# Performance work log

Measured on AMD Instinct MI355X. Metric: run time of the kernel, lower is better.

Reference implementation:

```python
import jax, jax.numpy as jnp
import numpy as np

D_MODEL = 4096
N_HEADS = 32
KV_HEADS = 8
HEAD_DIM = D_MODEL // N_HEADS  # 128
GROUPS = N_HEADS // KV_HEADS   # 4
ROPE_THETA = 500000.0
CLIP_QKV = 8.0
SEQLENS = [512, 768, 384, 384]
T = sum(SEQLENS)  # 2048 total ragged tokens


def setup_inputs() -> dict:
    key = jax.random.key(0)
    k1, k2, k3 = jax.random.split(key, 3)
    hidden_states = jax.random.normal(k1, (T, D_MODEL), dtype=jnp.float32)
    # fused Wqkv: rows = d_model (Q) + 2 * kv_heads * head_dim (K,V)
    w_qkv = jax.random.normal(k2, (D_MODEL + 2 * KV_HEADS * HEAD_DIM, D_MODEL), dtype=jnp.float32) * 0.02
    w_o = jax.random.normal(k3, (D_MODEL, D_MODEL), dtype=jnp.float32) * 0.02
    # ragged-batch metadata: cumulative sequence lengths, per-token positions
    cu = np.concatenate([[0], np.cumsum(SEQLENS)]).astype(np.int32)
    pos = np.concatenate([np.arange(l) for l in SEQLENS]).astype(np.float32)
    inv_freq = 1.0 / (ROPE_THETA ** (np.arange(0, HEAD_DIM, 2, dtype=np.float32) / HEAD_DIM))  # [64]
    freqs = pos[:, None] * inv_freq[None, :]  # [T, 64]
    return {
        "hidden_states": hidden_states,
        "w_qkv": w_qkv,
        "w_o": w_o,
        "cos": jnp.asarray(np.cos(freqs), dtype=jnp.float32),
        "sin": jnp.asarray(np.sin(freqs), dtype=jnp.float32),
        "cu_seqlens": jnp.asarray(cu),
    }


def _rope(x, cos, sin):
    # rotate-half (NeoX-style) RoPE, as in TGI PositionRotaryEmbedding
    h = HEAD_DIM // 2
    x1, x2 = x[..., :h], x[..., h:]
    c = cos[:, None, :]  # [T,1,h] broadcast over heads
    s = sin[:, None, :]
    return jnp.concatenate([x1 * c - x2 * s, x2 * c + x1 * s], axis=-1)


def reference(hidden_states, w_qkv, w_o, cos, sin, cu_seqlens):
    # fused QKV projection + clip_qkv clamp
    qkv = jnp.clip(hidden_states @ w_qkv.T, -CLIP_QKV, CLIP_QKV)  # [T, 6144]
    q_sz = N_HEADS * HEAD_DIM
    kv_sz = KV_HEADS * HEAD_DIM
    q = qkv[:, :q_sz].reshape(T, N_HEADS, HEAD_DIM)
    k = qkv[:, q_sz:q_sz + kv_sz].reshape(T, KV_HEADS, HEAD_DIM)
    v = qkv[:, q_sz + kv_sz:].reshape(T, KV_HEADS, HEAD_DIM)
    q = _rope(q, cos, sin)
    k = _rope(k, cos, sin)
    # GQA: expand kv heads to query heads (kv_head_mapping = repeat_interleave)
    kr = jnp.repeat(k, GROUPS, axis=1)  # [T, H, D]
    vr = jnp.repeat(v, GROUPS, axis=1)
    # varlen causal mask: same segment AND key index <= query index
    idx = jnp.arange(T)
    seg = jnp.searchsorted(cu_seqlens, idx, side="right") - 1  # [T]
    mask = (seg[:, None] == seg[None, :]) & (idx[:, None] >= idx[None, :])  # [T,T]
    scale = HEAD_DIM ** -0.5
    scores = jnp.einsum("qhd,khd->hqk", q, kr) * scale  # [H,T,T]
    scores = jnp.where(mask[None, :, :], scores, jnp.finfo(scores.dtype).min)
    attn = jax.nn.softmax(scores, axis=-1)
    out = jnp.einsum("hqk,khd->qhd", attn, vr).reshape(T, N_HEADS * HEAD_DIM)
    return out @ w_o.T
```

## Files before the change

### kernel.cpp

```cpp
#include <hip/hip_runtime.h>

#define T_TOK 2048
#define DM    4096
#define NH    32
#define KVH   8
#define HD    128
#define QKV_N 6144
#define KOFF  4096
#define VOFF  5120
#define SCALE 0.08838834764831845f

typedef __attribute__((ext_vector_type(8))) short  short8;
typedef __attribute__((ext_vector_type(4))) float  floatx4;

__device__ __forceinline__ ushort f2bf(float f) {
  union { float f; unsigned u; } x; x.f = f;
  unsigned u = x.u;
  return (ushort)((u + 0x7fffu + ((u >> 16) & 1u)) >> 16);
}
__device__ __forceinline__ float bf2f(ushort h) {
  union { unsigned u; float f; } x; x.u = ((unsigned)h) << 16;
  return x.f;
}

__global__ void __launch_bounds__(256) cast_bf16_kernel(const float* __restrict__ x,
                                                        ushort* __restrict__ y, int n4) {
  int i = blockIdx.x * 256 + threadIdx.x;
  if (i >= n4) return;
  float4 v = ((const float4*)x)[i];
  ushort4 o;
  o.x = f2bf(v.x); o.y = f2bf(v.y); o.z = f2bf(v.z); o.w = f2bf(v.w);
  ((ushort4*)y)[i] = o;
}

__global__ void __launch_bounds__(256) add_f32_kernel(const float4* __restrict__ a,
                                                      const float4* __restrict__ b,
                                                      float4* __restrict__ o, int n4) {
  int i = blockIdx.x * 256 + threadIdx.x;
  if (i >= n4) return;
  float4 x = a[i], y = b[i];
  o[i] = make_float4(x.x + y.x, x.y + y.y, x.z + y.z, x.w + y.w);
}

__device__ __forceinline__ void gld_lds16(const ushort* g, ushort* l) {
  __builtin_amdgcn_global_load_lds((const __attribute__((address_space(1))) unsigned int*)g,
                                   (__attribute__((address_space(3))) unsigned int*)l,
                                   16, 0, 0);
}

template <int MLO, int NLO>
__device__ __forceinline__ void mfma_quad(floatx4 (&acc)[8][4],
                                          const short8 (&afr)[4][2],
                                          const short8 (&bfr)[4][2]) {
  __builtin_amdgcn_s_setprio(1);
#pragma unroll
  for (int ks = 0; ks < 2; ++ks)
#pragma unroll
    for (int mi = 0; mi < 4; ++mi)
#pragma unroll
      for (int ni = 0; ni < 2; ++ni)
        acc[MLO + mi][NLO + ni] = __builtin_amdgcn_mfma_f32_16x16x32_bf16(
            afr[mi][ks], bfr[NLO + ni][ks], acc[MLO + mi][NLO + ni], 0, 0, 0);
  __builtin_amdgcn_s_setprio(0);
}

__device__ __forceinline__ void stage_half(const ushort* __restrict__ G, size_t row0,
                                           int K, int k0, ushort* lbase, int tid) {
#pragma unroll
  for (int j = 0; j < 2; ++j) {
    int row   = j * 64 + (tid >> 3);
    int chunk = (tid & 7) ^ (row & 7);
    gld_lds16(G + (row0 + (size_t)row) * K + k0 + chunk * 8,
              lbase + (size_t)(j * 512 + tid) * 8);
  }
}

#define TILE(BUF, tt)                                                             \
  do {                                                                            \
    const ushort* Ab = (BUF) ? Ab1 : Ab0;                                         \
    const ushort* Bb = (BUF) ? Bb1 : Bb0;                                         \
        \
    _Pragma("unroll") for (int ni = 0; ni < 2; ++ni)                              \
      _Pragma("unroll") for (int ks = 0; ks < 2; ++ks)                            \
        bfr[ni][ks] = *(const short8*)&Bb[(brow + ni * 16 + r) * 64 +             \
                                          ((ks * 32 + g * 8) ^ cswz)];            \
    _Pragma("unroll") for (int m = 0; m < 4; ++m)                                 \
      _Pragma("unroll") for (int ks = 0; ks < 2; ++ks)                            \
        afr[m][ks] = *(const short8*)&Ab[(m * 16 + r) * 64 +                      \
                                         ((ks * 32 + g * 8) ^ cswz)];             \
    if ((tt) + 1 < NT)                                                            \
      stage_half(A, bm + 128, K, koff + ((tt) + 1) * 64,                          \
                 &As[1 - (BUF)][1][0][0], tid);                                   \
    __builtin_amdgcn_s_barrier();                                                 \
    mfma_quad<0, 0>(acc, afr, bfr);                                               \
    __builtin_amdgcn_s_barrier();                                                 \
        \
    _Pragma("unroll") for (int ni = 2; ni < 4; ++ni)                              \
      _Pragma("unroll") for (int ks = 0; ks < 2; ++ks)                            \
        bfr[ni][ks] = *(const short8*)&Bb[(brow + ni * 16 + r) * 64 +             \
                                          ((ks * 32 + g * 8) ^ cswz)];            \
    __builtin_amdgcn_s_barrier();                                                 \
    mfma_quad<0, 2>(acc, afr, bfr);                                               \
    __builtin_amdgcn_s_barrier();                                                 \
        \
    _Pragma("unroll") for (int m = 0; m < 4; ++m)                                 \
      _Pragma("unroll") for (int ks = 0; ks < 2; ++ks)                            \
        afr[m][ks] = *(const short8*)&Ab[((64 + m * 16) + r) * 64 +               \
                                         ((ks * 32 + g * 8) ^ cswz)];             \
    if ((tt) + 2 < NT)                                                            \
      stage_half(B, bn, K, koff + ((tt) + 2) * 64, &Bs[BUF][0][0][0], tid);       \
    __builtin_amdgcn_s_barrier();                                                 \
    mfma_quad<4, 2>(acc, afr, bfr);                                               \
    __builtin_amdgcn_s_barrier();                                                 \
        \
    if ((tt) + 2 < NT) {                                                          \
      stage_half(B, bn + 128, K, koff + ((tt) + 2) * 64, &Bs[BUF][1][0][0], tid); \
      stage_half(A, bm, K, koff + ((tt) + 2) * 64, &As[BUF][0][0][0], tid);       \
    }                                                                             \
    if ((tt) < NT - 2) asm volatile("s_waitcnt vmcnt(6)");                        \
    else               asm volatile("s_waitcnt vmcnt(0)");                        \
    __builtin_amdgcn_s_barrier();                                                 \
    mfma_quad<4, 0>(acc, afr, bfr);                                               \
    __builtin_amdgcn_s_barrier();                                                 \
  } while (0)

__global__ void __launch_bounds__(512, 2)
gemm256(const ushort* __restrict__ A, const ushort* __restrict__ B,
        ushort* __restrict__ Cb, float* __restrict__ Cf,
        int N, int K, int Kloc, int KS, int mode) {
  __shared__ __align__(16) ushort As[2][2][128][64];
  __shared__ __align__(16) ushort Bs[2][2][128][64];

  const int tid = threadIdx.x;
  const int lane = tid & 63, wv = tid >> 6;
  const int r = lane & 15, g = lane >> 4;
  const int wm = wv >> 2, wn = wv & 3;

  const int nwg = (int)gridDim.x;
  const int wg  = (int)blockIdx.x;
  const int wgs = (wg & 7) * (nwg >> 3) + (wg >> 3);
  const int nbx = N >> 8;
  const int by  = wgs / (nbx * KS);
  const int rem = wgs - by * nbx * KS;
  const int bx  = rem / KS;
  const int ks_ = rem - bx * KS;
  const int bm = by * 256, bn = bx * 256;
  const int koff = ks_ * Kloc;

  const int NT = Kloc >> 6;

  floatx4 acc[8][4];
#pragma unroll
  for (int mi = 0; mi < 8; ++mi)
#pragma unroll
    for (int ni = 0; ni < 4; ++ni) acc[mi][ni] = (floatx4){0.f, 0.f, 0.f, 0.f};

  stage_half(B, bn,       K, koff, &Bs[0][0][0][0], tid);
  stage_half(B, bn + 128, K, koff, &Bs[0][1][0][0], tid);
  stage_half(A, bm,       K, koff, &As[0][0][0][0], tid);
  stage_half(A, bm + 128, K, koff, &As[0][1][0][0], tid);
  if (NT > 1) {
    stage_half(B, bn,       K, koff + 64, &Bs[1][0][0][0], tid);
    stage_half(B, bn + 128, K, koff + 64, &Bs[1][1][0][0], tid);
    stage_half(A, bm,       K, koff + 64, &As[1][0][0][0], tid);
    asm volatile("s_waitcnt vmcnt(6)");
  } else {
    asm volatile("s_waitcnt vmcnt(0)");
  }
  __builtin_amdgcn_s_barrier();

  short8 afr[4][2], bfr[4][2];
  const int cswz = (r & 7) << 3;
  const int brow = (wn & 1) * 64;
  const ushort* Ab0 = &As[0][wm][0][0];
  const ushort* Ab1 = &As[1][wm][0][0];
  const ushort* Bb0 = &Bs[0][wn >> 1][0][0];
  const ushort* Bb1 = &Bs[1][wn >> 1][0][0];

  for (int t = 0; t < NT; t += 2) {
    TILE(0, t);
    TILE(1, t + 1);
  }

  float* Cfo = Cf + (size_t)ks_ * ((size_t)2048 * N);
#pragma unroll
  for (int mi = 0; mi < 8; ++mi)
#pragma unroll
    for (int v = 0; v < 4; ++v) {
      int row = bm + wm * 128 + mi * 16 + g * 4 + v;
#pragma unroll
      for (int ni = 0; ni < 4; ++ni) {
        int col = bn + wn * 64 + ni * 16 + r;
        float x = acc[mi][ni][v];
        if (mode == 0) {
          x = fminf(8.0f, fmaxf(-8.0f, x));
          Cb[(size_t)row * N + col] = f2bf(x);
        } else {
          Cfo[(size_t)row * N + col] = x;
        }
      }
    }
}

__global__ void __launch_bounds__(256) rope_kernel(ushort* __restrict__ qkv,
                                                   const float* __restrict__ cosb,
                                                   const float* __restrict__ sinb) {
  int t = blockIdx.y;
  int h = blockIdx.x * 4 + (threadIdx.x >> 6);
  int d = threadIdx.x & 63;
  size_t base = (size_t)t * QKV_N + (h < NH ? h * HD : KOFF + (h - NH) * HD);
  float x1 = bf2f(qkv[base + d]);
  float x2 = bf2f(qkv[base + 64 + d]);
  float c = cosb[t * 64 + d], s = sinb[t * 64 + d];
  float y1 = x1 * c - x2 * s;
  float y2 = x2 * c + x1 * s;
  if (h < NH) { y1 *= SCALE; y2 *= SCALE; }
  qkv[base + d]      = f2bf(y1);
  qkv[base + 64 + d] = f2bf(y2);
}

__global__ void __launch_bounds__(256) vtrans_kernel(const ushort* __restrict__ qkv,
                                                     ushort* __restrict__ vt) {
  int idx = blockIdx.x * 256 + threadIdx.x;
  int t  = idx & (T_TOK - 1);
  int d  = (idx >> 11) & (HD - 1);
  int kv = idx >> 18;
  vt[idx] = qkv[(size_t)t * QKV_N + VOFF + kv * HD + d];
}

__global__ void __launch_bounds__(256) attn_kernel(const ushort* __restrict__ qkv,
                                                   const ushort* __restrict__ vt,
                                                   ushort* __restrict__ o) {
  __shared__ ushort Ks[64][136];
  __shared__ ushort Vts[128][72];
  __shared__ ushort Ps[4][16][72];

  const int tid = threadIdx.x, wave = tid >> 6, lane = tid & 63;
  const int r = lane & 15, g = lane >> 4;
  const int qtile = blockIdx.x, head = blockIdx.y, kvh = head >> 2;
  const int q0 = qtile * 64;
  int s0;
  if (q0 < 512) s0 = 0; else if (q0 < 1280) s0 = 512;
  else if (q0 < 1664) s0 = 1280; else s0 = 1664;

  short8 qf[4];
  const int qrow = q0 + wave * 16 + r;
#pragma unroll
  for (int ks = 0; ks < 4; ks++)
    qf[ks] = *(const short8*)&qkv[(size_t)qrow * QKV_N + head * HD + ks * 32 + g * 8];

  floatx4 zero = {0.f, 0.f, 0.f, 0.f};
  floatx4 oacc[8];
#pragma unroll
  for (int b = 0; b < 8; b++) oacc[b] = zero;
  float mrun[4] = {-1e30f, -1e30f, -1e30f, -1e30f};
  float lrun[4] = {0.f, 0.f, 0.f, 0.f};

  const size_t kcol  = (size_t)KOFF + kvh * HD;
  const size_t vbase = (size_t)kvh * HD * T_TOK;

  for (int k0 = s0; k0 < q0 + 64; k0 += 64) {
    short8 kreg[4], vreg[4];
#pragma unroll
    for (int p = 0; p < 4; p++) {
      int krow = p * 16 + (tid >> 4), kc = (tid & 15) * 8;
      kreg[p] = *(const short8*)&qkv[(size_t)(k0 + krow) * QKV_N + kcol + kc];
      int vd = p * 32 + (tid >> 3), vc = (tid & 7) * 8;
      vreg[p] = *(const short8*)&vt[vbase + (size_t)vd * T_TOK + k0 + vc];
    }
    __syncthreads();
#pragma unroll
    for (int p = 0; p < 4; p++) {
      int krow = p * 16 + (tid >> 4), kc = (tid & 15) * 8;
      *(short8*)&Ks[krow][kc] = kreg[p];
      int vd = p * 32 + (tid >> 3), vc = (tid & 7) * 8;
      *(short8*)&Vts[vd][vc] = vreg[p];
    }
    __syncthreads();

    floatx4 sacc[4];
#pragma unroll
    for (int s = 0; s < 4; s++) sacc[s] = zero;
#pragma unroll
    for (int s = 0; s < 4; s++)
#pragma unroll
      for (int ks = 0; ks < 4; ks++) {
        short8 kf = *(const short8*)&Ks[s * 16 + r][ks * 32 + g * 8];
        sacc[s] = __builtin_amdgcn_mfma_f32_16x16x32_bf16(qf[ks], kf, sacc[s], 0, 0, 0);
      }

    const bool diag = (k0 == q0);
    float sv[4][4];
#pragma unroll
    for (int s = 0; s < 4; s++)
#pragma unroll
      for (int v = 0; v < 4; v++) {
        float x = sacc[s][v];
        if (diag) {
          int ka = k0 + s * 16 + r;
          int qa = q0 + wave * 16 + g * 4 + v;
          if (ka > qa) x = -1e30f;
        }
        sv[s][v] = x;
      }

    float rmax[4];
#pragma unroll
    for (int v = 0; v < 4; v++)
      rmax[v] = fmaxf(fmaxf(sv[0][v], sv[1][v]), fmaxf(sv[2][v], sv[3][v]));
#pragma unroll
    for (int off = 1; off < 16; off <<= 1)
#pragma unroll
      for (int v = 0; v < 4; v++)
        rmax[v] = fmaxf(rmax[v], __shfl_xor(rmax[v], off, 64));

    float newm[4], alpha[4];
#pragma unroll
    for (int v = 0; v < 4; v++) {
      newm[v]  = fmaxf(mrun[v], rmax[v]);
      alpha[v] = __expf(mrun[v] - newm[v]);
      mrun[v]  = newm[v];
    }

    float pv[4][4];
    float rsum[4] = {0.f, 0.f, 0.f, 0.f};
#pragma unroll
    for (int s = 0; s < 4; s++)
#pragma unroll
      for (int v = 0; v < 4; v++) {
        float p = __expf(sv[s][v] - newm[v]);
        pv[s][v] = p;
        rsum[v] += p;
      }
#pragma unroll
    for (int off = 1; off < 16; off <<= 1)
#pragma unroll
      for (int v = 0; v < 4; v++)
        rsum[v] += __shfl_xor(rsum[v], off, 64);
#pragma unroll
    for (int v = 0; v < 4; v++) lrun[v] = lrun[v] * alpha[v] + rsum[v];
#pragma unroll
    for (int b = 0; b < 8; b++)
#pragma unroll
      for (int v = 0; v < 4; v++) oacc[b][v] *= alpha[v];

#pragma unroll
    for (int s = 0; s < 4; s++)
#pragma unroll
      for (int v = 0; v < 4; v++)
        Ps[wave][g * 4 + v][s * 16 + r] = f2bf(pv[s][v]);
    __syncthreads();

    short8 pf0 = *(const short8*)&Ps[wave][r][g * 8];
    short8 pf1 = *(const short8*)&Ps[wave][r][32 + g * 8];

#pragma unroll
    for (int b = 0; b < 8; b++) {
      short8 v0 = *(const short8*)&Vts[b * 16 + r][g * 8];
      short8 v1 = *(const short8*)&Vts[b * 16 + r][32 + g * 8];
      oacc[b] = __builtin_amdgcn_mfma_f32_16x16x32_bf16(pf0, v0, oacc[b], 0, 0, 0);
      oacc[b] = __builtin_amdgcn_mfma_f32_16x16x32_bf16(pf1, v1, oacc[b], 0, 0, 0);
    }
  }

  float rinv[4];
#pragma unroll
  for (int v = 0; v < 4; v++) rinv[v] = 1.0f / lrun[v];
#pragma unroll
  for (int b = 0; b < 8; b++)
#pragma unroll
    for (int v = 0; v < 4; v++) {
      int qa = q0 + wave * 16 + g * 4 + v;
      o[(size_t)qa * DM + head * HD + b * 16 + r] = f2bf(oacc[b][v] * rinv[v]);
    }
}

extern "C" void kernel_launch(void* const* d_in, const int* in_sizes, int n_in,
                              void* d_out, int out_size, void* d_ws, size_t ws_size,
                              hipStream_t stream) {
  const float* hs   = (const float*)d_in[0];
  const float* wqkv = (const float*)d_in[1];
  const float* wo   = (const float*)d_in[2];
  const float* cosb = (const float*)d_in[3];
  const float* sinb = (const float*)d_in[4];
  float* out = (float*)d_out;

  char* w = (char*)d_ws;
  ushort* h_bf   = (ushort*)(w);
  ushort* wq_bf  = (ushort*)(w + 16777216);
  ushort* wo_bf  = (ushort*)(w + 67108864);
  ushort* qkv_bf = (ushort*)(w + 100663296);
  ushort* vt     = (ushort*)(w + 125829120);
  ushort* ao_bf  = (ushort*)(w + 130023424);
  float*  part   = (float*)(w);

  cast_bf16_kernel<<<8192,  256, 0, stream>>>(hs,   h_bf,  2097152);
  cast_bf16_kernel<<<24576, 256, 0, stream>>>(wqkv, wq_bf, 6291456);
  cast_bf16_kernel<<<16384, 256, 0, stream>>>(wo,   wo_bf, 4194304);

  gemm256<<<dim3(192), 512, 0, stream>>>(h_bf, wq_bf, qkv_bf, nullptr,
                                         QKV_N, DM, DM, 1, 0);
  rope_kernel<<<dim3(10, T_TOK), 256, 0, stream>>>(qkv_bf, cosb, sinb);
  vtrans_kernel<<<8192, 256, 0, stream>>>(qkv_bf, vt);
  attn_kernel<<<dim3(32, 32), 256, 0, stream>>>(qkv_bf, vt, ao_bf);
  gemm256<<<dim3(256), 512, 0, stream>>>(ao_bf, wo_bf, nullptr, part,
                                         DM, DM, 2048, 2, 1);
  add_f32_kernel<<<8192, 256, 0, stream>>>((const float4*)part,
                                           (const float4*)(part + (size_t)2048 * 4096),
                                           (float4*)out, 2097152);
}
```

Baseline: 550.6 us.

## Restructure GEMM LDS pipeline with cross-tile fragment prefetch; prefetch attention K/V

```diff
diff --git a/kernel.cpp b/kernel.cpp
--- a/kernel.cpp
+++ b/kernel.cpp
@@ -49,9 +49,9 @@
 }
 
 template <int MLO, int NLO>
-__device__ __forceinline__ void mfma_quad(floatx4 (&acc)[8][4],
-                                          const short8 (&afr)[4][2],
-                                          const short8 (&bfr)[4][2]) {
+__device__ __forceinline__ void mfma_q(floatx4 (&acc)[8][4],
+                                       const short8 (&a)[4][2],
+                                       const short8 (&b)[2][2]) {
   __builtin_amdgcn_s_setprio(1);
 #pragma unroll
   for (int ks = 0; ks < 2; ++ks)
@@ -60,7 +60,7 @@
 #pragma unroll
       for (int ni = 0; ni < 2; ++ni)
         acc[MLO + mi][NLO + ni] = __builtin_amdgcn_mfma_f32_16x16x32_bf16(
-            afr[mi][ks], bfr[NLO + ni][ks], acc[MLO + mi][NLO + ni], 0, 0, 0);
+            a[mi][ks], b[ni][ks], acc[MLO + mi][NLO + ni], 0, 0, 0);
   __builtin_amdgcn_s_setprio(0);
 }
 
@@ -75,52 +75,50 @@
   }
 }
 
-#define TILE(BUF, tt)                                                             \
+#define TILE_P(P, tt)                                                             \
   do {                                                                            \
-    const ushort* Ab = (BUF) ? Ab1 : Ab0;                                         \
-    const ushort* Bb = (BUF) ? Bb1 : Bb0;                                         \
-        \
+    const ushort* AbC = (P) ? Ab1 : Ab0;                                          \
+    const ushort* BbC = (P) ? Bb1 : Bb0;                                          \
+    const ushort* AbN = (P) ? Ab0 : Ab1;                                          \
+    const ushort* BbN = (P) ? Bb0 : Bb1;                                          \
+    int t2 = (tt) + 2; if (t2 >= NT) t2 = NT - 1;                                 \
+    const int k2 = koff + t2 * 64;                                                \
+                                  \
     _Pragma("unroll") for (int ni = 0; ni < 2; ++ni)                              \
       _Pragma("unroll") for (int ks = 0; ks < 2; ++ks)                            \
-        bfr[ni][ks] = *(const short8*)&Bb[(brow + ni * 16 + r) * 64 +             \
-                                          ((ks * 32 + g * 8) ^ cswz)];            \
-    _Pragma("unroll") for (int m = 0; m < 4; ++m)                                 \
-      _Pragma("unroll") for (int ks = 0; ks < 2; ++ks)                            \
-        afr[m][ks] = *(const short8*)&Ab[(m * 16 + r) * 64 +                      \
-                                         ((ks * 32 + g * 8) ^ cswz)];             \
-    if ((tt) + 1 < NT)                                                            \
-      stage_half(A, bm + 128, K, koff + ((tt) + 1) * 64,                          \
-                 &As[1 - (BUF)][1][0][0], tid);                                   \
-    __builtin_amdgcn_s_barrier();                                                 \
-    mfma_quad<0, 0>(acc, afr, bfr);                                               \
-    __builtin_amdgcn_s_barrier();                                                 \
-        \
-    _Pragma("unroll") for (int ni = 2; ni < 4; ++ni)                              \
-      _Pragma("unroll") for (int ks = 0; ks < 2; ++ks)                            \
-        bfr[ni][ks] = *(const short8*)&Bb[(brow + ni * 16 + r) * 64 +             \
-                                          ((ks * 32 + g * 8) ^ cswz)];            \
-    __builtin_amdgcn_s_barrier();                                                 \
-    mfma_quad<0, 2>(acc, afr, bfr);                                               \
+        bhi[ni][ks] = *(const short8*)&BbC[(brow + 32 + ni * 16 + r) * 64 +       \
+                                           ((ks * 32 + g * 8) ^ cswz)];           \
+    __builtin_amdgcn_s_barrier();                                                 \
+    mfma_q<0, 0>(acc, alo, blo);                                                  \
     __builtin_amdgcn_s_barrier();                                                 \
         \
     _Pragma("unroll") for (int m = 0; m < 4; ++m)                                 \
       _Pragma("unroll") for (int ks = 0; ks < 2; ++ks)                            \
-        afr[m][ks] = *(const short8*)&Ab[((64 + m * 16) + r) * 64 +               \
-                                         ((ks * 32 + g * 8) ^ cswz)];             \
-    if ((tt) + 2 < NT)                                                            \
-      stage_half(B, bn, K, koff + ((tt) + 2) * 64, &Bs[BUF][0][0][0], tid);       \
-    __builtin_amdgcn_s_barrier();                                                 \
-    mfma_quad<4, 2>(acc, afr, bfr);                                               \
-    __builtin_amdgcn_s_barrier();                                                 \
-        \
-    if ((tt) + 2 < NT) {                                                          \
-      stage_half(B, bn + 128, K, koff + ((tt) + 2) * 64, &Bs[BUF][1][0][0], tid); \
-      stage_half(A, bm, K, koff + ((tt) + 2) * 64, &As[BUF][0][0][0], tid);       \
-    }                                                                             \
-    if ((tt) < NT - 2) asm volatile("s_waitcnt vmcnt(6)");                        \
-    else               asm volatile("s_waitcnt vmcnt(0)");                        \
-    __builtin_amdgcn_s_barrier();                                                 \
-    mfma_quad<4, 0>(acc, afr, bfr);                                               \
+        ahi[m][ks] = *(const short8*)&AbC[((64 + m * 16) + r) * 64 +              \
+                                          ((ks * 32 + g * 8) ^ cswz)];            \
+    __builtin_amdgcn_s_barrier();                                                 \
+    mfma_q<0, 2>(acc, alo, bhi);                                                  \
+    asm volatile("s_waitcnt vmcnt(0)");                                           \
+    __builtin_amdgcn_s_barrier();                                                 \
+       \
+    _Pragma("unroll") for (int m = 0; m < 4; ++m)                                 \
+      _Pragma("unroll") for (int ks = 0; ks < 2; ++ks)                            \
+        alo[m][ks] = *(const short8*)&AbN[(m * 16 + r) * 64 +                     \
+                                          ((ks * 32 + g * 8) ^ cswz)];            \
+    stage_half(B, bn,       K, k2, &Bs[P][0][0][0], tid);                         \
+    stage_half(B, bn + 128, K, k2, &Bs[P][1][0][0], tid);                         \
+    __builtin_amdgcn_s_barrier();                                                 \
+    mfma_q<4, 2>(acc, ahi, bhi);                                                  \
+    __builtin_amdgcn_s_barrier();                                                 \
+             \
+    stage_half(A, bm,       K, k2, &As[P][0][0][0], tid);                         \
+    stage_half(A, bm + 128, K, k2, &As[P][1][0][0], tid);                         \
+    __builtin_amdgcn_s_barrier();                                                 \
+    mfma_q<4, 0>(acc, ahi, blo);                                                  \
+    _Pragma("unroll") for (int ni = 0; ni < 2; ++ni)                              \
+      _Pragma("unroll") for (int ks = 0; ks < 2; ++ks)                            \
+        blo[ni][ks] = *(const short8*)&BbN[(brow + ni * 16 + r) * 64 +            \
+                                           ((ks * 32 + g * 8) ^ cswz)];           \
     __builtin_amdgcn_s_barrier();                                                 \
   } while (0)
 
@@ -155,21 +153,18 @@
 #pragma unroll
     for (int ni = 0; ni < 4; ++ni) acc[mi][ni] = (floatx4){0.f, 0.f, 0.f, 0.f};
 
-  stage_half(B, bn,       K, koff, &Bs[0][0][0][0], tid);
-  stage_half(B, bn + 128, K, koff, &Bs[0][1][0][0], tid);
-  stage_half(A, bm,       K, koff, &As[0][0][0][0], tid);
-  stage_half(A, bm + 128, K, koff, &As[0][1][0][0], tid);
-  if (NT > 1) {
-    stage_half(B, bn,       K, koff + 64, &Bs[1][0][0][0], tid);
-    stage_half(B, bn + 128, K, koff + 64, &Bs[1][1][0][0], tid);
-    stage_half(A, bm,       K, koff + 64, &As[1][0][0][0], tid);
-    asm volatile("s_waitcnt vmcnt(6)");
-  } else {
-    asm volatile("s_waitcnt vmcnt(0)");
-  }
+  stage_half(B, bn,       K, koff,      &Bs[0][0][0][0], tid);
+  stage_half(B, bn + 128, K, koff,      &Bs[0][1][0][0], tid);
+  stage_half(A, bm,       K, koff,      &As[0][0][0][0], tid);
+  stage_half(A, bm + 128, K, koff,      &As[0][1][0][0], tid);
+  stage_half(B, bn,       K, koff + 64, &Bs[1][0][0][0], tid);
+  stage_half(B, bn + 128, K, koff + 64, &Bs[1][1][0][0], tid);
+  stage_half(A, bm,       K, koff + 64, &As[1][0][0][0], tid);
+  stage_half(A, bm + 128, K, koff + 64, &As[1][1][0][0], tid);
+  asm volatile("s_waitcnt vmcnt(8)");
   __builtin_amdgcn_s_barrier();
 
-  short8 afr[4][2], bfr[4][2];
+  short8 alo[4][2], ahi[4][2], blo[2][2], bhi[2][2];
   const int cswz = (r & 7) << 3;
   const int brow = (wn & 1) * 64;
   const ushort* Ab0 = &As[0][wm][0][0];
@@ -177,9 +172,20 @@
   const ushort* Bb0 = &Bs[0][wn >> 1][0][0];
   const ushort* Bb1 = &Bs[1][wn >> 1][0][0];
 
+#pragma unroll
+  for (int m = 0; m < 4; ++m)
+#pragma unroll
+    for (int ks = 0; ks < 2; ++ks)
+      alo[m][ks] = *(const short8*)&Ab0[(m * 16 + r) * 64 + ((ks * 32 + g * 8) ^ cswz)];
+#pragma unroll
+  for (int ni = 0; ni < 2; ++ni)
+#pragma unroll
+    for (int ks = 0; ks < 2; ++ks)
+      blo[ni][ks] = *(const short8*)&Bb0[(brow + ni * 16 + r) * 64 + ((ks * 32 + g * 8) ^ cswz)];
+
   for (int t = 0; t < NT; t += 2) {
-    TILE(0, t);
-    TILE(1, t + 1);
+    TILE_P(0, t);
+    TILE_P(1, t + 1);
   }
 
   float* Cfo = Cf + (size_t)ks_ * ((size_t)2048 * N);
@@ -259,15 +265,16 @@
   const size_t kcol  = (size_t)KOFF + kvh * HD;
   const size_t vbase = (size_t)kvh * HD * T_TOK;
 
+  short8 kreg[4], vreg[4];
+#pragma unroll
+  for (int p = 0; p < 4; p++) {
+    int krow = p * 16 + (tid >> 4), kc = (tid & 15) * 8;
+    kreg[p] = *(const short8*)&qkv[(size_t)(s0 + krow) * QKV_N + kcol + kc];
+    int vd = p * 32 + (tid >> 3), vc = (tid & 7) * 8;
+    vreg[p] = *(const short8*)&vt[vbase + (size_t)vd * T_TOK + s0 + vc];
+  }
+
   for (int k0 = s0; k0 < q0 + 64; k0 += 64) {
-    short8 kreg[4], vreg[4];
-#pragma unroll
-    for (int p = 0; p < 4; p++) {
-      int krow = p * 16 + (tid >> 4), kc = (tid & 15) * 8;
-      kreg[p] = *(const short8*)&qkv[(size_t)(k0 + krow) * QKV_N + kcol + kc];
-      int vd = p * 32 + (tid >> 3), vc = (tid & 7) * 8;
-      vreg[p] = *(const short8*)&vt[vbase + (size_t)vd * T_TOK + k0 + vc];
-    }
     __syncthreads();
 #pragma unroll
     for (int p = 0; p < 4; p++) {
@@ -277,6 +284,17 @@
       *(short8*)&Vts[vd][vc] = vreg[p];
     }
     __syncthreads();
+
+    if (k0 < q0) {
+      int kn = k0 + 64;
+#pragma unroll
+      for (int p = 0; p < 4; p++) {
+        int krow = p * 16 + (tid >> 4), kc = (tid & 15) * 8;
+        kreg[p] = *(const short8*)&qkv[(size_t)(kn + krow) * QKV_N + kcol + kc];
+        int vd = p * 32 + (tid >> 3), vc = (tid & 7) * 8;
+        vreg[p] = *(const short8*)&vt[vbase + (size_t)vd * T_TOK + kn + vc];
+      }
+    }
 
     floatx4 sacc[4];
 #pragma unroll
@@ -349,7 +367,6 @@
 #pragma unroll
       for (int v = 0; v < 4; v++)
         Ps[wave][g * 4 + v][s * 16 + r] = f2bf(pv[s][v]);
-    __syncthreads();
 
     short8 pf0 = *(const short8*)&Ps[wave][r][g * 8];
     short8 pf1 = *(const short8*)&Ps[wave][r][32 + g * 8];
```

New measurement: 609.7 us. 10.7% more time.
